# Kernel optimization log

Hardware: AMD Instinct MI355X
Metric: run time of the kernel (lower is better)

## Reference

```python
import jax, jax.numpy as jnp
import numpy as np

H, C = 2, 32  # heads, out_channels per head
NEG_SLOPE = 0.2


def gatv2_layer(h, src, dst, ea, W, b, We, att, bias, N):
    # shared lin_l = lin_r (share_weights=True)
    z = (h @ W + b).reshape(N, H, C)                      # [N,H,C]
    e = (ea @ We).reshape(-1, H, C)                        # [E',H,C]
    s = jax.nn.leaky_relu(z[dst] + z[src] + e, NEG_SLOPE)  # [E',H,C]
    alpha = jnp.einsum('ehc,hc->eh', s, att)               # [E',H]
    # segment softmax over destination neighborhoods
    m = jax.ops.segment_max(alpha, dst, num_segments=N)
    m = jnp.where(jnp.isfinite(m), m, 0.0)
    ex = jnp.exp(alpha - m[dst])
    denom = jax.ops.segment_sum(ex, dst, num_segments=N)
    a = ex / (denom[dst] + 1e-16)                          # [E',H]
    msg = (z[src] * a[:, :, None]).reshape(-1, H * C)      # [E',H*C]
    out = jax.ops.segment_sum(msg, dst, num_segments=N) + bias
    return out                                             # [N,H*C]


def setup_inputs() -> dict:
    key = jax.random.key(0)
    ks = jax.random.split(key, 16)
    N, E = 50000, 800000
    inp = {
        'x': jax.random.normal(ks[0], (N, 2), jnp.float32),
        'edge_index': jax.random.randint(ks[1], (2, E), 0, N, jnp.int64 if jax.config.jax_enable_x64 else jnp.int32).astype(jnp.int32),
        'edge_attr': jax.random.uniform(ks[2], (E, 2), jnp.float32),
        'dest_index': 123,
        'W0': jax.random.normal(ks[3], (2, 64), jnp.float32) * 0.5,
        'b0': jnp.zeros((64,), jnp.float32),
        'We0': jax.random.normal(ks[4], (2, 64), jnp.float32) * 0.5,
        'att0': jax.random.normal(ks[5], (H, C), jnp.float32) * 0.5,
        'bias0': jnp.zeros((64,), jnp.float32),
        'W1': jax.random.normal(ks[6], (64, 64), jnp.float32) * 0.125,
        'b1': jnp.zeros((64,), jnp.float32),
        'We1': jax.random.normal(ks[7], (2, 64), jnp.float32) * 0.5,
        'att1': jax.random.normal(ks[8], (H, C), jnp.float32) * 0.5,
        'bias1': jnp.zeros((64,), jnp.float32),
        'Wm1': jax.random.normal(ks[9], (194, 32), jnp.float32) * 0.07,
        'bm1': jnp.zeros((32,), jnp.float32),
        'Wm2': jax.random.normal(ks[10], (32, 1), jnp.float32) * 0.17,
        'bm2': jnp.zeros((1,), jnp.float32),
    }
    return inp


def reference(x, edge_index, edge_attr, dest_index,
              W0, b0, We0, att0, bias0,
              W1, b1, We1, att1, bias1,
              Wm1, bm1, Wm2, bm2):
    N = x.shape[0]
    # add self loops (fill_value='mean' for edge_attr)
    loops = jnp.arange(N, dtype=edge_index.dtype)
    src = jnp.concatenate([edge_index[0], loops])
    dst = jnp.concatenate([edge_index[1], loops])
    ea_sl = jnp.concatenate(
        [edge_attr, jnp.broadcast_to(edge_attr.mean(axis=0), (N, edge_attr.shape[1]))], axis=0)

    h = x
    h = jax.nn.elu(gatv2_layer(h, src, dst, ea_sl, W0, b0, We0, att0, bias0, N))
    h = jax.nn.elu(gatv2_layer(h, src, dst, ea_sl, W1, b1, We1, att1, bias1, N))

    goal = h[dest_index]                                   # [64]
    src_emb = h[edge_index[0]]                             # [E,64]
    dst_emb = h[edge_index[1]]                             # [E,64]
    goal_rep = jnp.broadcast_to(goal, (edge_index.shape[1], goal.shape[0]))
    edge_in = jnp.concatenate([src_emb, dst_emb, goal_rep, edge_attr], axis=-1)  # [E,194]
    hmlp = jax.nn.relu(edge_in @ Wm1 + bm1)
    logits = (hmlp @ Wm2 + bm2).squeeze(-1)                # [E]
    return logits
```

## Files before the change

### kernel.cpp

```cpp
#include <hip/hip_runtime.h>
#include <hip/hip_bf16.h>
#include <math.h>


typedef __attribute__((ext_vector_type(8))) short short8;
typedef __attribute__((ext_vector_type(4))) float f32x4;

#define BSH 7
#define CH 4096

template <int IMM>
__device__ __forceinline__ float swz(float x) {
    return __int_as_float(__builtin_amdgcn_ds_swizzle(__float_as_int(x), IMM));
}

template <int CTRL>
__device__ __forceinline__ float dpp_add(float p) {
    int t = __builtin_amdgcn_update_dpp(0, __float_as_int(p), CTRL, 0xF, 0xF, true);
    return p + __int_as_float(t);
}

__device__ __forceinline__ float head_reduce(float p) {
    p = dpp_add<0xB1>(p);
    p = dpp_add<0x4E>(p);
    p = dpp_add<0x141>(p);
    p = dpp_add<0x140>(p);
    p += swz<0x401F>(p);
    return p;
}

__device__ __forceinline__ short2 bsplit(float x) {
    unsigned u = __float_as_uint(x);
    short hi = (short)(u >> 16);
    float hif = __uint_as_float(u & 0xFFFF0000u);
    short lo = (short)(__float_as_uint(x - hif) >> 16);
    return make_short2(hi, lo);
}

__global__ void init_kernel(int* __restrict__ bucket_base, float* __restrict__ easum,
                            int nbuck) {
    int i = blockIdx.x * blockDim.x + threadIdx.x;
    if (i < nbuck) bucket_base[i] = 0;
    if (i < 2) easum[i] = 0.f;
}

__global__ __launch_bounds__(256) void easum_kernel(const float2* __restrict__ ea,
                                                    float* __restrict__ easum, int E) {
    __shared__ float r0[4], r1[4];
    int stride = gridDim.x * blockDim.x;
    float s0 = 0.f, s1 = 0.f;
    for (int e = blockIdx.x * blockDim.x + threadIdx.x; e < E; e += stride) {
        float2 v = ea[e];
        s0 += v.x; s1 += v.y;
    }
#pragma unroll
    for (int o = 32; o >= 1; o >>= 1) {
        s0 += __shfl_xor(s0, o);
        s1 += __shfl_xor(s1, o);
    }
    int wave = threadIdx.x >> 6;
    if ((threadIdx.x & 63) == 0) { r0[wave] = s0; r1[wave] = s1; }
    __syncthreads();
    if (threadIdx.x == 0) {
        atomicAdd(&easum[0], r0[0] + r0[1] + r0[2] + r0[3]);
        atomicAdd(&easum[1], r1[0] + r1[1] + r1[2] + r1[3]);
    }
}

__global__ __launch_bounds__(256) void bhist_kernel(const int* __restrict__ ei,
                                                    int* __restrict__ bucket_base,
                                                    int E, int EP, int nbuck) {
    extern __shared__ int lcnt[];
    int tid = threadIdx.x;
    for (int i = tid; i < nbuck; i += 256) lcnt[i] = 0;
    __syncthreads();
    int base = blockIdx.x * CH;
    int end = min(base + CH, EP);
    for (int i = base + tid; i < end; i += 256) {
        int d = (i < E) ? ei[E + i] : (i - E);
        atomicAdd(&lcnt[d >> BSH], 1);
    }
    __syncthreads();
    for (int i = tid; i < nbuck; i += 256) {
        int c = lcnt[i];
        if (c) atomicAdd(&bucket_base[i], c);
    }
}

__global__ __launch_bounds__(256) void bscan_kernel(int* __restrict__ bucket_base,
                                                    int* __restrict__ bucket_cursor,
                                                    int* __restrict__ row_ptr,
                                                    int N, int nbuck) {
    __shared__ int sm[256];
    int tid = threadIdx.x;
    int K = (nbuck + 255) / 256;
    int b0 = tid * K;
    int local = 0;
    for (int k = 0; k < K; ++k) {
        int b = b0 + k;
        if (b < nbuck) local += bucket_base[b];
    }
    sm[tid] = local;
    __syncthreads();
    for (int st = 1; st < 256; st <<= 1) {
        int v = sm[tid];
        int a = (tid >= st) ? sm[tid - st] : 0;
        __syncthreads();
        sm[tid] = v + a;
        __syncthreads();
    }
    int run = (tid == 0) ? 0 : sm[tid - 1];
    for (int k = 0; k < K; ++k) {
        int b = b0 + k;
        if (b < nbuck) {
            int c = bucket_base[b];
            bucket_base[b] = run;
            bucket_cursor[b] = run;
            run += c;
        }
    }
    if (tid == 255) {
        bucket_base[nbuck] = sm[255];
        row_ptr[N] = sm[255];
    }
}

__global__ __launch_bounds__(256) void phaseA_kernel(const int* __restrict__ ei,
                                                     const float2* __restrict__ ea,
                                                     const float* __restrict__ easum,
                                                     int* __restrict__ bucket_cursor,
                                                     float4* __restrict__ staged,
                                                     int E, int EP, int nbuck) {
    extern __shared__ int sm[];
    int* lcnt = sm;
    int* lbase = sm + nbuck;
    int tid = threadIdx.x;
    for (int i = tid; i < nbuck; i += 256) lcnt[i] = 0;
    __syncthreads();
    int base = blockIdx.x * CH;
    int end = min(base + CH, EP);
    for (int i = base + tid; i < end; i += 256) {
        int d = (i < E) ? ei[E + i] : (i - E);
        atomicAdd(&lcnt[d >> BSH], 1);
    }
    __syncthreads();
    for (int i = tid; i < nbuck; i += 256) {
        int c = lcnt[i];
        lbase[i] = c ? atomicAdd(&bucket_cursor[i], c) : 0;
        lcnt[i] = 0;
    }
    __syncthreads();
    float inv = 1.f / (float)E;
    float m0 = easum[0] * inv, m1 = easum[1] * inv;
    for (int i = base + tid; i < end; i += 256) {
        int s, d; float ex, ey;
        if (i < E) {
            s = ei[i]; d = ei[E + i];
            float2 v = ea[i]; ex = v.x; ey = v.y;
        } else {
            s = d = i - E; ex = m0; ey = m1;
        }
        int b = d >> BSH;
        int pos = lbase[b] + atomicAdd(&lcnt[b], 1);
        staged[pos] = make_float4(__int_as_float(s), ex, ey, __int_as_float(d));
    }
}

__global__ __launch_bounds__(256) void phaseB_kernel(const float4* __restrict__ staged,
                                                     const int* __restrict__ bucket_base,
                                                     int* __restrict__ row_ptr,
                                                     float4* __restrict__ recs, int N) {
    __shared__ int cnt128[128];
    __shared__ int offs[128];
    int b = blockIdx.x;
    int n0 = b << BSH;
    int tid = threadIdx.x;
    if (tid < 128) cnt128[tid] = 0;
    __syncthreads();
    int begs = bucket_base[b];
    int ends = bucket_base[b + 1];
    for (int i = begs + tid; i < ends; i += 256) {
        int d = __float_as_int(staged[i].w);
        atomicAdd(&cnt128[d - n0], 1);
    }
    __syncthreads();
    if (tid < 128) offs[tid] = cnt128[tid];
    __syncthreads();
    for (int st = 1; st < 128; st <<= 1) {
        int v = 0;
        if (tid < 128) {
            v = offs[tid];
            if (tid >= st) v += offs[tid - st];
        }
        __syncthreads();
        if (tid < 128) offs[tid] = v;
        __syncthreads();
    }
    if (tid < 128) {
        int excl = begs + offs[tid] - cnt128[tid];
        int node = n0 + tid;
        if (node < N) row_ptr[node] = excl;
        offs[tid] = excl;
    }
    __syncthreads();
    for (int i = begs + tid; i < ends; i += 256) {
        float4 r = staged[i];
        int d = __float_as_int(r.w);
        int pos = atomicAdd(&offs[d - n0], 1);
        recs[pos] = r;
    }
}

__global__ __launch_bounds__(512) void bfrag_kernel(const float* __restrict__ W1,
                                                    const float* __restrict__ Wm1,
                                                    short* __restrict__ BfW1,
                                                    short* __restrict__ BfWm) {
    int snt = threadIdx.x >> 6;
    int lane = threadIdx.x & 63;
    int s = snt >> 2, nt = snt & 3;
    int col = nt * 16 + (lane & 15);
    short* Bf = blockIdx.x == 0 ? BfW1 : BfWm;
#pragma unroll
    for (int j = 0; j < 8; ++j) {
        int k = s * 32 + (lane >> 4) * 8 + j;
        float v;
        if (blockIdx.x == 0) {
            v = W1[k * 64 + col];
        } else {
            v = (col < 32) ? Wm1[k * 32 + col] : Wm1[(64 + k) * 32 + (col - 32)];
        }
        short2 t = bsplit(v);
        Bf[(snt * 2 + 0) * 512 + lane * 8 + j] = t.x;
        Bf[(snt * 2 + 1) * 512 + lane * 8 + j] = t.y;
    }
}

__global__ __launch_bounds__(256) void mfma_gemm64(const float* __restrict__ h,
                                                   const short* __restrict__ Bf,
                                                   const float* __restrict__ bias,
                                                   float* __restrict__ out, int N) {
    int wave = threadIdx.x >> 6;
    int lane = threadIdx.x & 63;
    int n0 = blockIdx.x * 64 + wave * 16;
    if (n0 >= N) return;
    int m = lane & 15, quad = lane >> 4;
    int arow = n0 + m;
    if (arow > N - 1) arow = N - 1;

    f32x4 acc[4] = {{0.f, 0.f, 0.f, 0.f}, {0.f, 0.f, 0.f, 0.f},
                    {0.f, 0.f, 0.f, 0.f}, {0.f, 0.f, 0.f, 0.f}};
#pragma unroll
    for (int s = 0; s < 2; ++s) {
        const float* ap = h + (size_t)arow * 64 + s * 32 + quad * 8;
        float4 a0 = *(const float4*)ap;
        float4 a1 = *(const float4*)(ap + 4);
        short8 ahi, alo;
        short2 t;
        t = bsplit(a0.x); ahi[0] = t.x; alo[0] = t.y;
        t = bsplit(a0.y); ahi[1] = t.x; alo[1] = t.y;
        t = bsplit(a0.z); ahi[2] = t.x; alo[2] = t.y;
        t = bsplit(a0.w); ahi[3] = t.x; alo[3] = t.y;
        t = bsplit(a1.x); ahi[4] = t.x; alo[4] = t.y;
        t = bsplit(a1.y); ahi[5] = t.x; alo[5] = t.y;
        t = bsplit(a1.z); ahi[6] = t.x; alo[6] = t.y;
        t = bsplit(a1.w); ahi[7] = t.x; alo[7] = t.y;
#pragma unroll
        for (int nt = 0; nt < 4; ++nt) {
            const short* bp = Bf + ((s * 4 + nt) * 2) * 512 + lane * 8;
            short8 bhi = *(const short8*)bp;
            short8 blo = *(const short8*)(bp + 512);
            acc[nt] = __builtin_amdgcn_mfma_f32_16x16x32_bf16(ahi, bhi, acc[nt], 0, 0, 0);
            acc[nt] = __builtin_amdgcn_mfma_f32_16x16x32_bf16(ahi, blo, acc[nt], 0, 0, 0);
            acc[nt] = __builtin_amdgcn_mfma_f32_16x16x32_bf16(alo, bhi, acc[nt], 0, 0, 0);
        }
    }
#pragma unroll
    for (int nt = 0; nt < 4; ++nt) {
        int col = nt * 16 + m;
        float bj = bias ? bias[col] : 0.f;
#pragma unroll
        for (int r = 0; r < 4; ++r) {
            int orow = n0 + quad * 4 + r;
            if (orow < N) out[(size_t)orow * 64 + col] = acc[nt][r] + bj;
        }
    }
}

__global__ __launch_bounds__(256) void agg0_kernel(
    const float2* __restrict__ x, const float* __restrict__ W0,
    const float* __restrict__ b0, const int* __restrict__ row_ptr,
    const float4* __restrict__ recs,
    const float* __restrict__ We, const float* __restrict__ att,
    const float* __restrict__ bias, float* __restrict__ hout, int N) {
    int gtid = blockIdx.x * blockDim.x + threadIdx.x;
    int n = gtid >> 6;
    if (n >= N) return;
    n = __builtin_amdgcn_readfirstlane(n);
    int lane = threadIdx.x & 63;

    float W0a = W0[lane], W0b = W0[64 + lane], b0c = b0[lane];
    float We0 = We[lane], We1 = We[64 + lane];
    float attj = att[lane];
    float2 xn = x[n];
    float zn = fmaf(xn.x, W0a, fmaf(xn.y, W0b, b0c));

    int beg = row_ptr[n], end = row_ptr[n + 1];
    float ll[4] = {0.f, 0.f, 0.f, 0.f};
    float aa[4] = {0.f, 0.f, 0.f, 0.f};
    int i = beg;
    for (; i + 7 < end; i += 8) {
        float w[8], zsv[8];
#pragma unroll
        for (int k = 0; k < 8; ++k) {
            float4 r = recs[i + k];
            int s = __builtin_amdgcn_readfirstlane(__float_as_int(r.x));
            float2 xs = x[s];
            float zs = fmaf(xs.x, W0a, fmaf(xs.y, W0b, b0c));
            float sj = zn + zs + fmaf(r.y, We0, r.z * We1);
            sj = fmaxf(sj, 0.2f * sj);
            float alpha = head_reduce(sj * attj);
            w[k] = __expf(fminf(alpha, 60.f));
            zsv[k] = zs;
        }
#pragma unroll
        for (int k = 0; k < 8; ++k) {
            ll[k & 3] += w[k];
            aa[k & 3] = fmaf(w[k], zsv[k], aa[k & 3]);
        }
    }
    for (; i < end; ++i) {
        float4 r = recs[i];
        int s = __builtin_amdgcn_readfirstlane(__float_as_int(r.x));
        float2 xs = x[s];
        float zs = fmaf(xs.x, W0a, fmaf(xs.y, W0b, b0c));
        float sj = zn + zs + fmaf(r.y, We0, r.z * We1);
        sj = fmaxf(sj, 0.2f * sj);
        float alpha = head_reduce(sj * attj);
        float w = __expf(fminf(alpha, 60.f));
        ll[0] += w;
        aa[0] = fmaf(w, zs, aa[0]);
    }
    float l = (ll[0] + ll[1]) + (ll[2] + ll[3]);
    float acc = (aa[0] + aa[1]) + (aa[2] + aa[3]);
    float v = acc / (l + 1e-16f) + bias[lane];
    v = (v > 0.f) ? v : expm1f(v);
    hout[n * 64 + lane] = v;
}

__global__ __launch_bounds__(256) void agg1_kernel(
    const float* __restrict__ z, const int* __restrict__ row_ptr,
    const float4* __restrict__ recs,
    const float* __restrict__ We, const float* __restrict__ att,
    const float* __restrict__ bias, float* __restrict__ hout, int N) {
    int gtid = blockIdx.x * blockDim.x + threadIdx.x;
    int n = gtid >> 6;
    if (n >= N) return;
    n = __builtin_amdgcn_readfirstlane(n);
    int lane = threadIdx.x & 63;

    float We0 = We[lane], We1 = We[64 + lane];
    float attj = att[lane];
    float zn = z[n * 64 + lane];

    int beg = row_ptr[n], end = row_ptr[n + 1];
    float ll[4] = {0.f, 0.f, 0.f, 0.f};
    float aa[4] = {0.f, 0.f, 0.f, 0.f};
    int i = beg;
    for (; i + 7 < end; i += 8) {
        float w[8], zsv[8];
#pragma unroll
        for (int k = 0; k < 8; ++k) {
            float4 r = recs[i + k];
            int s = __builtin_amdgcn_readfirstlane(__float_as_int(r.x));
            float zs = z[s * 64 + lane];
            float sj = zn + zs + fmaf(r.y, We0, r.z * We1);
            sj = fmaxf(sj, 0.2f * sj);
            float alpha = head_reduce(sj * attj);
            w[k] = __expf(fminf(alpha, 60.f));
            zsv[k] = zs;
        }
#pragma unroll
        for (int k = 0; k < 8; ++k) {
            ll[k & 3] += w[k];
            aa[k & 3] = fmaf(w[k], zsv[k], aa[k & 3]);
        }
    }
    for (; i < end; ++i) {
        float4 r = recs[i];
        int s = __builtin_amdgcn_readfirstlane(__float_as_int(r.x));
        float zs = z[s * 64 + lane];
        float sj = zn + zs + fmaf(r.y, We0, r.z * We1);
        sj = fmaxf(sj, 0.2f * sj);
        float alpha = head_reduce(sj * attj);
        float w = __expf(fminf(alpha, 60.f));
        ll[0] += w;
        aa[0] = fmaf(w, zs, aa[0]);
    }
    float l = (ll[0] + ll[1]) + (ll[2] + ll[3]);
    float acc = (aa[0] + aa[1]) + (aa[2] + aa[3]);
    float v = acc / (l + 1e-16f) + bias[lane];
    v = (v > 0.f) ? v : expm1f(v);
    hout[n * 64 + lane] = v;
}

__global__ void gvec_kernel(const float* __restrict__ h, const float* __restrict__ Wm1,
                            const float* __restrict__ bm1, const int* __restrict__ dest,
                            float* __restrict__ gvec) {
    int q = threadIdx.x;
    if (q >= 32) return;
    int d = dest[0];
    float acc = bm1[q];
    for (int k = 0; k < 64; ++k)
        acc = fmaf(h[d * 64 + k], Wm1[(128 + k) * 32 + q], acc);
    gvec[q] = acc;
}

__global__ __launch_bounds__(256) void edge_mlp_kernel(
    const int* __restrict__ ei, const float2* __restrict__ ea,
    const float* __restrict__ hsd, const float* __restrict__ gvec,
    const float* __restrict__ WrowA, const float* __restrict__ WrowB,
    const float* __restrict__ Wm2, const float* __restrict__ bm2,
    float* __restrict__ out, int E) {
    int tid = blockIdx.x * blockDim.x + threadIdx.x;
    int e = tid >> 3;
    int j = tid & 7;
    if (e >= E) return;
    int s = ei[e], d = ei[E + e];
    float2 eav = ea[e];
    float4 a = *(const float4*)(hsd + (size_t)s * 64 + j * 4);
    float4 bv = *(const float4*)(hsd + (size_t)d * 64 + 32 + j * 4);
    float4 g = *(const float4*)(gvec + j * 4);
    float4 wa = *(const float4*)(WrowA + j * 4);
    float4 wb = *(const float4*)(WrowB + j * 4);
    float4 w2 = *(const float4*)(Wm2 + j * 4);
    float acc = 0.f, v;
    v = fmaf(eav.x, wa.x, fmaf(eav.y, wb.x, a.x + bv.x + g.x)); v = fmaxf(v, 0.f); acc = fmaf(v, w2.x, acc);
    v = fmaf(eav.x, wa.y, fmaf(eav.y, wb.y, a.y + bv.y + g.y)); v = fmaxf(v, 0.f); acc = fmaf(v, w2.y, acc);
    v = fmaf(eav.x, wa.z, fmaf(eav.y, wb.z, a.z + bv.z + g.z)); v = fmaxf(v, 0.f); acc = fmaf(v, w2.z, acc);
    v = fmaf(eav.x, wa.w, fmaf(eav.y, wb.w, a.w + bv.w + g.w)); v = fmaxf(v, 0.f); acc = fmaf(v, w2.w, acc);
    acc = dpp_add<0xB1>(acc);
    acc = dpp_add<0x4E>(acc);
    acc = dpp_add<0x141>(acc);
    if (j == 0) out[e] = acc + bm2[0];
}

extern "C" void kernel_launch(void* const* d_in, const int* in_sizes, int n_in,
                              void* d_out, int out_size, void* d_ws, size_t ws_size,
                              hipStream_t stream) {
    const float* x     = (const float*)d_in[0];
    const int*   ei    = (const int*)d_in[1];
    const float* ea    = (const float*)d_in[2];
    const int*   dest  = (const int*)d_in[3];
    const float* W0    = (const float*)d_in[4];
    const float* b0    = (const float*)d_in[5];
    const float* We0   = (const float*)d_in[6];
    const float* att0  = (const float*)d_in[7];
    const float* bias0 = (const float*)d_in[8];
    const float* W1    = (const float*)d_in[9];
    const float* b1    = (const float*)d_in[10];
    const float* We1   = (const float*)d_in[11];
    const float* att1  = (const float*)d_in[12];
    const float* bias1 = (const float*)d_in[13];
    const float* Wm1   = (const float*)d_in[14];
    const float* bm1   = (const float*)d_in[15];
    const float* Wm2   = (const float*)d_in[16];
    const float* bm2   = (const float*)d_in[17];

    const int N = in_sizes[0] / 2;
    const int E = in_sizes[1] / 2;
    const int EP = E + N;
    const int nbuck = (N + 127) >> BSH;
    const int nchunk = (EP + CH - 1) / CH;

    char* ws = (char*)d_ws;
    size_t off = 0;
    auto alloc = [&](size_t bytes) -> void* {
        void* p = ws + off;
        off += bytes;
        off = (off + 255) & ~(size_t)255;
        return p;
    };
    int*    bucket_base   = (int*)alloc((size_t)(nbuck + 1) * 4);
    int*    bucket_cursor = (int*)alloc((size_t)nbuck * 4);
    int*    row_ptr       = (int*)alloc((size_t)(N + 1) * 4);
    size_t  shared_bytes  = (size_t)EP * 16 > (size_t)N * 256 ? (size_t)EP * 16
                                                              : (size_t)N * 256;
    float4* staged        = (float4*)alloc(shared_bytes);
    float4* recs          = (float4*)alloc((size_t)EP * 16);
    float*  hbuf          = (float*)alloc((size_t)N * 64 * 4);
    float*  easum         = (float*)alloc(8);
    float*  gvec          = (float*)alloc(32 * 4);
    short*  BfW1          = (short*)alloc(8192 * 2);
    short*  BfWm          = (short*)alloc(8192 * 2);
    float*  zbuf          = (float*)staged;
    float*  hsd           = zbuf;

    dim3 blk(256);
    init_kernel<<<(nbuck + 255) / 256, blk, 0, stream>>>(bucket_base, easum, nbuck);
    easum_kernel<<<128, blk, 0, stream>>>((const float2*)ea, easum, E);
    bhist_kernel<<<nchunk, blk, (size_t)nbuck * 4, stream>>>(ei, bucket_base, E, EP, nbuck);
    bscan_kernel<<<1, blk, 0, stream>>>(bucket_base, bucket_cursor, row_ptr, N, nbuck);
    phaseA_kernel<<<nchunk, blk, (size_t)nbuck * 8, stream>>>(ei, (const float2*)ea, easum,
                                                              bucket_cursor, staged, E, EP, nbuck);
    phaseB_kernel<<<nbuck, blk, 0, stream>>>(staged, bucket_base, row_ptr, recs, N);
    bfrag_kernel<<<2, 512, 0, stream>>>(W1, Wm1, BfW1, BfWm);
    agg0_kernel<<<(N * 64 + 255) / 256, blk, 0, stream>>>((const float2*)x, W0, b0,
                                                          row_ptr, recs,
                                                          We0, att0, bias0, hbuf, N);
    mfma_gemm64<<<(N + 63) / 64, blk, 0, stream>>>(hbuf, BfW1, b1, zbuf, N);
    agg1_kernel<<<(N * 64 + 255) / 256, blk, 0, stream>>>(zbuf, row_ptr, recs,
                                                          We1, att1, bias1, hbuf, N);
    gvec_kernel<<<1, 64, 0, stream>>>(hbuf, Wm1, bm1, dest, gvec);
    mfma_gemm64<<<(N + 63) / 64, blk, 0, stream>>>(hbuf, BfWm, (const float*)nullptr, hsd, N);
    edge_mlp_kernel<<<((size_t)E * 8 + 255) / 256, blk, 0, stream>>>(
        ei, (const float2*)ea, hsd, gvec,
        Wm1 + 192 * 32, Wm1 + 193 * 32, Wm2, bm2, (float*)d_out, E);
}
```

Before: 293.0 us.

## Precompute per-edge attention weights in edge-parallel kernels and fuse setup launches

```diff
diff --git a/kernel.cpp b/kernel.cpp
--- a/kernel.cpp
+++ b/kernel.cpp
@@ -18,15 +18,6 @@
 __device__ __forceinline__ float dpp_add(float p) {
     int t = __builtin_amdgcn_update_dpp(0, __float_as_int(p), CTRL, 0xF, 0xF, true);
     return p + __int_as_float(t);
-}
-
-__device__ __forceinline__ float head_reduce(float p) {
-    p = dpp_add<0xB1>(p);
-    p = dpp_add<0x4E>(p);
-    p = dpp_add<0x141>(p);
-    p = dpp_add<0x140>(p);
-    p += swz<0x401F>(p);
-    return p;
 }
 
 __device__ __forceinline__ short2 bsplit(float x) {
@@ -37,19 +28,49 @@
     return make_short2(hi, lo);
 }
 
-__global__ void init_kernel(int* __restrict__ bucket_base, float* __restrict__ easum,
-                            int nbuck) {
-    int i = blockIdx.x * blockDim.x + threadIdx.x;
-    if (i < nbuck) bucket_base[i] = 0;
-    if (i < 2) easum[i] = 0.f;
-}
-
-__global__ __launch_bounds__(256) void easum_kernel(const float2* __restrict__ ea,
-                                                    float* __restrict__ easum, int E) {
+__global__ __launch_bounds__(512) void setup_kernel(const float* __restrict__ W1,
+                                                    const float* __restrict__ Wm1,
+                                                    short* __restrict__ BfW1,
+                                                    short* __restrict__ BfWm,
+                                                    int* __restrict__ bucket_base,
+                                                    float* __restrict__ easum, int nbuck) {
+    if (blockIdx.x == 2) {
+        for (int i = threadIdx.x; i <= nbuck; i += 512) bucket_base[i] = 0;
+        if (threadIdx.x < 2) easum[threadIdx.x] = 0.f;
+        return;
+    }
+    int snt = threadIdx.x >> 6;
+    int lane = threadIdx.x & 63;
+    int s = snt >> 2, nt = snt & 3;
+    int col = nt * 16 + (lane & 15);
+    short* Bf = blockIdx.x == 0 ? BfW1 : BfWm;
+#pragma unroll
+    for (int j = 0; j < 8; ++j) {
+        int k = s * 32 + (lane >> 4) * 8 + j;
+        float v;
+        if (blockIdx.x == 0) {
+            v = W1[k * 64 + col];
+        } else {
+            v = (col < 32) ? Wm1[k * 32 + col] : Wm1[(64 + k) * 32 + (col - 32)];
+        }
+        short2 t = bsplit(v);
+        Bf[(snt * 2 + 0) * 512 + lane * 8 + j] = t.x;
+        Bf[(snt * 2 + 1) * 512 + lane * 8 + j] = t.y;
+    }
+}
+
+__global__ __launch_bounds__(256) void pre_kernel(const int* __restrict__ ei,
+                                                  const float2* __restrict__ ea,
+                                                  int* __restrict__ bucket_base,
+                                                  float* __restrict__ easum,
+                                                  int E, int EP, int nbuck) {
+    extern __shared__ int lcnt[];
     __shared__ float r0[4], r1[4];
-    int stride = gridDim.x * blockDim.x;
+    int tid = threadIdx.x;
+    for (int i = tid; i < nbuck; i += 256) lcnt[i] = 0;
     float s0 = 0.f, s1 = 0.f;
-    for (int e = blockIdx.x * blockDim.x + threadIdx.x; e < E; e += stride) {
+    int estride = gridDim.x * 256;
+    for (int e = blockIdx.x * 256 + tid; e < E; e += estride) {
         float2 v = ea[e];
         s0 += v.x; s1 += v.y;
     }
@@ -58,21 +79,8 @@
         s0 += __shfl_xor(s0, o);
         s1 += __shfl_xor(s1, o);
     }
-    int wave = threadIdx.x >> 6;
-    if ((threadIdx.x & 63) == 0) { r0[wave] = s0; r1[wave] = s1; }
-    __syncthreads();
-    if (threadIdx.x == 0) {
-        atomicAdd(&easum[0], r0[0] + r0[1] + r0[2] + r0[3]);
-        atomicAdd(&easum[1], r1[0] + r1[1] + r1[2] + r1[3]);
-    }
-}
-
-__global__ __launch_bounds__(256) void bhist_kernel(const int* __restrict__ ei,
-                                                    int* __restrict__ bucket_base,
-                                                    int E, int EP, int nbuck) {
-    extern __shared__ int lcnt[];
-    int tid = threadIdx.x;
-    for (int i = tid; i < nbuck; i += 256) lcnt[i] = 0;
+    int wave = tid >> 6;
+    if ((tid & 63) == 0) { r0[wave] = s0; r1[wave] = s1; }
     __syncthreads();
     int base = blockIdx.x * CH;
     int end = min(base + CH, EP);
@@ -81,6 +89,10 @@
         atomicAdd(&lcnt[d >> BSH], 1);
     }
     __syncthreads();
+    if (tid == 0) {
+        atomicAdd(&easum[0], r0[0] + r0[1] + r0[2] + r0[3]);
+        atomicAdd(&easum[1], r1[0] + r1[1] + r1[2] + r1[3]);
+    }
     for (int i = tid; i < nbuck; i += 256) {
         int c = lcnt[i];
         if (c) atomicAdd(&bucket_base[i], c);
@@ -211,208 +223,269 @@
     }
 }
 
-__global__ __launch_bounds__(512) void bfrag_kernel(const float* __restrict__ W1,
-                                                    const float* __restrict__ Wm1,
-                                                    short* __restrict__ BfW1,
-                                                    short* __restrict__ BfWm) {
-    int snt = threadIdx.x >> 6;
+__global__ __launch_bounds__(256) void wgt1_kernel(const float* __restrict__ z,
+                                                   const float4* __restrict__ recs,
+                                                   const float* __restrict__ We,
+                                                   const float* __restrict__ att,
+                                                   float4* __restrict__ wbuf, int EP) {
     int lane = threadIdx.x & 63;
-    int s = snt >> 2, nt = snt & 3;
-    int col = nt * 16 + (lane & 15);
-    short* Bf = blockIdx.x == 0 ? BfW1 : BfWm;
+    int m = lane & 15, quad = lane >> 4;
+    int c0 = quad * 8, c1 = 32 + c0;
+    float w0a[8], w1a[8], ata[8], w0b[8], w1b[8], atb[8];
 #pragma unroll
     for (int j = 0; j < 8; ++j) {
-        int k = s * 32 + (lane >> 4) * 8 + j;
-        float v;
-        if (blockIdx.x == 0) {
-            v = W1[k * 64 + col];
-        } else {
-            v = (col < 32) ? Wm1[k * 32 + col] : Wm1[(64 + k) * 32 + (col - 32)];
-        }
-        short2 t = bsplit(v);
-        Bf[(snt * 2 + 0) * 512 + lane * 8 + j] = t.x;
-        Bf[(snt * 2 + 1) * 512 + lane * 8 + j] = t.y;
-    }
-}
-
-__global__ __launch_bounds__(256) void mfma_gemm64(const float* __restrict__ h,
-                                                   const short* __restrict__ Bf,
-                                                   const float* __restrict__ bias,
-                                                   float* __restrict__ out, int N) {
-    int wave = threadIdx.x >> 6;
+        w0a[j] = We[c0 + j];  w1a[j] = We[64 + c0 + j];  ata[j] = att[c0 + j];
+        w0b[j] = We[c1 + j];  w1b[j] = We[64 + c1 + j];  atb[j] = att[c1 + j];
+    }
+    int ntiles = (EP + 15) >> 4;
+    int wid = (blockIdx.x * blockDim.x + threadIdx.x) >> 6;
+    int nw = (gridDim.x * blockDim.x) >> 6;
+    for (int t = wid; t < ntiles; t += nw) {
+        int e = t * 16 + m;
+        int ec = e < EP ? e : EP - 1;
+        float4 r = recs[ec];
+        int s = __float_as_int(r.x);
+        int d = __float_as_int(r.w);
+        const float* zs = z + (size_t)s * 64;
+        const float* zd = z + (size_t)d * 64;
+        float4 sa0 = *(const float4*)(zs + c0), sa1 = *(const float4*)(zs + c0 + 4);
+        float4 sb0 = *(const float4*)(zs + c1), sb1 = *(const float4*)(zs + c1 + 4);
+        float4 da0 = *(const float4*)(zd + c0), da1 = *(const float4*)(zd + c0 + 4);
+        float4 db0 = *(const float4*)(zd + c1), db1 = *(const float4*)(zd + c1 + 4);
+        float sva[8] = {sa0.x, sa0.y, sa0.z, sa0.w, sa1.x, sa1.y, sa1.z, sa1.w};
+        float svb[8] = {sb0.x, sb0.y, sb0.z, sb0.w, sb1.x, sb1.y, sb1.z, sb1.w};
+        float dva[8] = {da0.x, da0.y, da0.z, da0.w, da1.x, da1.y, da1.z, da1.w};
+        float dvb[8] = {db0.x, db0.y, db0.z, db0.w, db1.x, db1.y, db1.z, db1.w};
+        float P0 = 0.f, P1 = 0.f;
+#pragma unroll
+        for (int j = 0; j < 8; ++j) {
+            float t0 = dva[j] + sva[j] + fmaf(r.y, w0a[j], r.z * w1a[j]);
+            t0 = fmaxf(t0, 0.2f * t0);
+            P0 = fmaf(t0, ata[j], P0);
+            float t1 = dvb[j] + svb[j] + fmaf(r.y, w0b[j], r.z * w1b[j]);
+            t1 = fmaxf(t1, 0.2f * t1);
+            P1 = fmaf(t1, atb[j], P1);
+        }
+        P0 += swz<0x401F>(P0);
+        P1 += swz<0x401F>(P1);
+        P0 += __shfl_xor(P0, 32);
+        P1 += __shfl_xor(P1, 32);
+        float w0 = __expf(fminf(P0, 60.f));
+        float w1 = __expf(fminf(P1, 60.f));
+        if (lane < 16 && e < EP) wbuf[e] = make_float4(w0, w1, r.x, 0.f);
+    }
+}
+
+__global__ __launch_bounds__(256) void wgt0_kernel(const float2* __restrict__ x,
+                                                   const float* __restrict__ W0,
+                                                   const float* __restrict__ b0,
+                                                   const float4* __restrict__ recs,
+                                                   const float* __restrict__ We,
+                                                   const float* __restrict__ att,
+                                                   float4* __restrict__ wbuf, int EP) {
     int lane = threadIdx.x & 63;
-    int n0 = blockIdx.x * 64 + wave * 16;
-    if (n0 >= N) return;
     int m = lane & 15, quad = lane >> 4;
-    int arow = n0 + m;
-    if (arow > N - 1) arow = N - 1;
-
-    f32x4 acc[4] = {{0.f, 0.f, 0.f, 0.f}, {0.f, 0.f, 0.f, 0.f},
-                    {0.f, 0.f, 0.f, 0.f}, {0.f, 0.f, 0.f, 0.f}};
-#pragma unroll
-    for (int s = 0; s < 2; ++s) {
-        const float* ap = h + (size_t)arow * 64 + s * 32 + quad * 8;
-        float4 a0 = *(const float4*)ap;
-        float4 a1 = *(const float4*)(ap + 4);
-        short8 ahi, alo;
-        short2 t;
-        t = bsplit(a0.x); ahi[0] = t.x; alo[0] = t.y;
-        t = bsplit(a0.y); ahi[1] = t.x; alo[1] = t.y;
-        t = bsplit(a0.z); ahi[2] = t.x; alo[2] = t.y;
-        t = bsplit(a0.w); ahi[3] = t.x; alo[3] = t.y;
-        t = bsplit(a1.x); ahi[4] = t.x; alo[4] = t.y;
-        t = bsplit(a1.y); ahi[5] = t.x; alo[5] = t.y;
-        t = bsplit(a1.z); ahi[6] = t.x; alo[6] = t.y;
-        t = bsplit(a1.w); ahi[7] = t.x; alo[7] = t.y;
-#pragma unroll
-        for (int nt = 0; nt < 4; ++nt) {
-            const short* bp = Bf + ((s * 4 + nt) * 2) * 512 + lane * 8;
-            short8 bhi = *(const short8*)bp;
-            short8 blo = *(const short8*)(bp + 512);
-            acc[nt] = __builtin_amdgcn_mfma_f32_16x16x32_bf16(ahi, bhi, acc[nt], 0, 0, 0);
-            acc[nt] = __builtin_amdgcn_mfma_f32_16x16x32_bf16(ahi, blo, acc[nt], 0, 0, 0);
-            acc[nt] = __builtin_amdgcn_mfma_f32_16x16x32_bf16(alo, bhi, acc[nt], 0, 0, 0);
-        }
-    }
-#pragma unroll
-    for (int nt = 0; nt < 4; ++nt) {
-        int col = nt * 16 + m;
-        float bj = bias ? bias[col] : 0.f;
-#pragma unroll
-        for (int r = 0; r < 4; ++r) {
-            int orow = n0 + quad * 4 + r;
-            if (orow < N) out[(size_t)orow * 64 + col] = acc[nt][r] + bj;
-        }
-    }
-}
-
-__global__ __launch_bounds__(256) void agg0_kernel(
-    const float2* __restrict__ x, const float* __restrict__ W0,
-    const float* __restrict__ b0, const int* __restrict__ row_ptr,
-    const float4* __restrict__ recs,
-    const float* __restrict__ We, const float* __restrict__ att,
-    const float* __restrict__ bias, float* __restrict__ hout, int N) {
+    int c0 = quad * 8, c1 = 32 + c0;
+    float w0a[8], w1a[8], ata[8], w0b[8], w1b[8], atb[8];
+    float Wxa[8], Wya[8], bca[8], Wxb[8], Wyb[8], bcb[8];
+#pragma unroll
+    for (int j = 0; j < 8; ++j) {
+        w0a[j] = We[c0 + j];  w1a[j] = We[64 + c0 + j];  ata[j] = att[c0 + j];
+        w0b[j] = We[c1 + j];  w1b[j] = We[64 + c1 + j];  atb[j] = att[c1 + j];
+        Wxa[j] = W0[c0 + j];  Wya[j] = W0[64 + c0 + j];  bca[j] = b0[c0 + j];
+        Wxb[j] = W0[c1 + j];  Wyb[j] = W0[64 + c1 + j];  bcb[j] = b0[c1 + j];
+    }
+    int ntiles = (EP + 15) >> 4;
+    int wid = (blockIdx.x * blockDim.x + threadIdx.x) >> 6;
+    int nw = (gridDim.x * blockDim.x) >> 6;
+    for (int t = wid; t < ntiles; t += nw) {
+        int e = t * 16 + m;
+        int ec = e < EP ? e : EP - 1;
+        float4 r = recs[ec];
+        int s = __float_as_int(r.x);
+        int d = __float_as_int(r.w);
+        float2 xs = x[s];
+        float2 xd = x[d];
+        float P0 = 0.f, P1 = 0.f;
+#pragma unroll
+        for (int j = 0; j < 8; ++j) {
+            float zs = fmaf(xs.x, Wxa[j], fmaf(xs.y, Wya[j], bca[j]));
+            float zd = fmaf(xd.x, Wxa[j], fmaf(xd.y, Wya[j], bca[j]));
+            float t0 = zd + zs + fmaf(r.y, w0a[j], r.z * w1a[j]);
+            t0 = fmaxf(t0, 0.2f * t0);
+            P0 = fmaf(t0, ata[j], P0);
+            float zs1 = fmaf(xs.x, Wxb[j], fmaf(xs.y, Wyb[j], bcb[j]));
+            float zd1 = fmaf(xd.x, Wxb[j], fmaf(xd.y, Wyb[j], bcb[j]));
+            float t1 = zd1 + zs1 + fmaf(r.y, w0b[j], r.z * w1b[j]);
+            t1 = fmaxf(t1, 0.2f * t1);
+            P1 = fmaf(t1, atb[j], P1);
+        }
+        P0 += swz<0x401F>(P0);
+        P1 += swz<0x401F>(P1);
+        P0 += __shfl_xor(P0, 32);
+        P1 += __shfl_xor(P1, 32);
+        float w0 = __expf(fminf(P0, 60.f));
+        float w1 = __expf(fminf(P1, 60.f));
+        if (lane < 16 && e < EP) wbuf[e] = make_float4(w0, w1, r.x, 0.f);
+    }
+}
+
+__global__ __launch_bounds__(256) void aggw1_kernel(const float* __restrict__ z,
+                                                    const int* __restrict__ row_ptr,
+                                                    const float4* __restrict__ wbuf,
+                                                    const float* __restrict__ bias,
+                                                    float* __restrict__ hout, int N) {
     int gtid = blockIdx.x * blockDim.x + threadIdx.x;
     int n = gtid >> 6;
     if (n >= N) return;
     n = __builtin_amdgcn_readfirstlane(n);
     int lane = threadIdx.x & 63;
-
-    float W0a = W0[lane], W0b = W0[64 + lane], b0c = b0[lane];
-    float We0 = We[lane], We1 = We[64 + lane];
-    float attj = att[lane];
-    float2 xn = x[n];
-    float zn = fmaf(xn.x, W0a, fmaf(xn.y, W0b, b0c));
-
+    int head = lane >> 5;
     int beg = row_ptr[n], end = row_ptr[n + 1];
     float ll[4] = {0.f, 0.f, 0.f, 0.f};
     float aa[4] = {0.f, 0.f, 0.f, 0.f};
     int i = beg;
-    for (; i + 7 < end; i += 8) {
-        float w[8], zsv[8];
+    for (; i + 8 <= end; i += 8) {
+        float w[8], zs[8];
 #pragma unroll
         for (int k = 0; k < 8; ++k) {
-            float4 r = recs[i + k];
-            int s = __builtin_amdgcn_readfirstlane(__float_as_int(r.x));
-            float2 xs = x[s];
-            float zs = fmaf(xs.x, W0a, fmaf(xs.y, W0b, b0c));
-            float sj = zn + zs + fmaf(r.y, We0, r.z * We1);
-            sj = fmaxf(sj, 0.2f * sj);
-            float alpha = head_reduce(sj * attj);
-            w[k] = __expf(fminf(alpha, 60.f));
-            zsv[k] = zs;
+            float4 r = wbuf[i + k];
+            int s = __builtin_amdgcn_readfirstlane(__float_as_int(r.z));
+            w[k] = head ? r.y : r.x;
+            zs[k] = z[(size_t)s * 64 + lane];
         }
 #pragma unroll
         for (int k = 0; k < 8; ++k) {
             ll[k & 3] += w[k];
-            aa[k & 3] = fmaf(w[k], zsv[k], aa[k & 3]);
+            aa[k & 3] = fmaf(w[k], zs[k], aa[k & 3]);
         }
     }
     for (; i < end; ++i) {
-        float4 r = recs[i];
-        int s = __builtin_amdgcn_readfirstlane(__float_as_int(r.x));
-        float2 xs = x[s];
-        float zs = fmaf(xs.x, W0a, fmaf(xs.y, W0b, b0c));
-        float sj = zn + zs + fmaf(r.y, We0, r.z * We1);
-        sj = fmaxf(sj, 0.2f * sj);
-        float alpha = head_reduce(sj * attj);
-        float w = __expf(fminf(alpha, 60.f));
+        float4 r = wbuf[i];
+        int s = __builtin_amdgcn_readfirstlane(__float_as_int(r.z));
+        float w = head ? r.y : r.x;
+        float zs = z[(size_t)s * 64 + lane];
         ll[0] += w;
         aa[0] = fmaf(w, zs, aa[0]);
     }
     float l = (ll[0] + ll[1]) + (ll[2] + ll[3]);
-    float acc = (aa[0] + aa[1]) + (aa[2] + aa[3]);
-    float v = acc / (l + 1e-16f) + bias[lane];
+    float a = (aa[0] + aa[1]) + (aa[2] + aa[3]);
+    float v = a / (l + 1e-16f) + bias[lane];
     v = (v > 0.f) ? v : expm1f(v);
-    hout[n * 64 + lane] = v;
-}
-
-__global__ __launch_bounds__(256) void agg1_kernel(
-    const float* __restrict__ z, const int* __restrict__ row_ptr,
-    const float4* __restrict__ recs,
-    const float* __restrict__ We, const float* __restrict__ att,
-    const float* __restrict__ bias, float* __restrict__ hout, int N) {
+    hout[(size_t)n * 64 + lane] = v;
+}
+
+__global__ __launch_bounds__(256) void aggw0_kernel(const float2* __restrict__ x,
+                                                    const float* __restrict__ W0,
+                                                    const float* __restrict__ b0,
+                                                    const int* __restrict__ row_ptr,
+                                                    const float4* __restrict__ wbuf,
+                                                    const float* __restrict__ bias,
+                                                    float* __restrict__ hout, int N) {
     int gtid = blockIdx.x * blockDim.x + threadIdx.x;
     int n = gtid >> 6;
     if (n >= N) return;
     n = __builtin_amdgcn_readfirstlane(n);
     int lane = threadIdx.x & 63;
-
-    float We0 = We[lane], We1 = We[64 + lane];
-    float attj = att[lane];
-    float zn = z[n * 64 + lane];
-
+    int head = lane >> 5;
+    float W0a = W0[lane], W0b = W0[64 + lane], b0c = b0[lane];
     int beg = row_ptr[n], end = row_ptr[n + 1];
     float ll[4] = {0.f, 0.f, 0.f, 0.f};
     float aa[4] = {0.f, 0.f, 0.f, 0.f};
     int i = beg;
-    for (; i + 7 < end; i += 8) {
-        float w[8], zsv[8];
+    for (; i + 8 <= end; i += 8) {
+        float w[8], zs[8];
 #pragma unroll
         for (int k = 0; k < 8; ++k) {
-            float4 r = recs[i + k];
-            int s = __builtin_amdgcn_readfirstlane(__float_as_int(r.x));
-            float zs = z[s * 64 + lane];
-            float sj = zn + zs + fmaf(r.y, We0, r.z * We1);
-            sj = fmaxf(sj, 0.2f * sj);
-            float alpha = head_reduce(sj * attj);
-            w[k] = __expf(fminf(alpha, 60.f));
-            zsv[k] = zs;
+            float4 r = wbuf[i + k];
+            int s = __builtin_amdgcn_readfirstlane(__float_as_int(r.z));
+            float2 xs = x[s];
+            w[k] = head ? r.y : r.x;
+            zs[k] = fmaf(xs.x, W0a, fmaf(xs.y, W0b, b0c));
         }
 #pragma unroll
         for (int k = 0; k < 8; ++k) {
             ll[k & 3] += w[k];
-            aa[k & 3] = fmaf(w[k], zsv[k], aa[k & 3]);
+            aa[k & 3] = fmaf(w[k], zs[k], aa[k & 3]);
         }
     }
     for (; i < end; ++i) {
-        float4 r = recs[i];
-        int s = __builtin_amdgcn_readfirstlane(__float_as_int(r.x));
-        float zs = z[s * 64 + lane];
-        float sj = zn + zs + fmaf(r.y, We0, r.z * We1);
-        sj = fmaxf(sj, 0.2f * sj);
-        float alpha = head_reduce(sj * attj);
-        float w = __expf(fminf(alpha, 60.f));
+        float4 r = wbuf[i];
+        int s = __builtin_amdgcn_readfirstlane(__float_as_int(r.z));
+        float2 xs = x[s];
+        float w = head ? r.y : r.x;
+        float zs = fmaf(xs.x, W0a, fmaf(xs.y, W0b, b0c));
         ll[0] += w;
         aa[0] = fmaf(w, zs, aa[0]);
     }
     float l = (ll[0] + ll[1]) + (ll[2] + ll[3]);
-    float acc = (aa[0] + aa[1]) + (aa[2] + aa[3]);
-    float v = acc / (l + 1e-16f) + bias[lane];
+    float a = (aa[0] + aa[1]) + (aa[2] + aa[3]);
+    float v = a / (l + 1e-16f) + bias[lane];
     v = (v > 0.f) ? v : expm1f(v);
-    hout[n * 64 + lane] = v;
-}
-
-__global__ void gvec_kernel(const float* __restrict__ h, const float* __restrict__ Wm1,
-                            const float* __restrict__ bm1, const int* __restrict__ dest,
-                            float* __restrict__ gvec) {
-    int q = threadIdx.x;
-    if (q >= 32) return;
-    int d = dest[0];
-    float acc = bm1[q];
-    for (int k = 0; k < 64; ++k)
-        acc = fmaf(h[d * 64 + k], Wm1[(128 + k) * 32 + q], acc);
-    gvec[q] = acc;
+    hout[(size_t)n * 64 + lane] = v;
+}
+
+__global__ __launch_bounds__(256) void mfma_gemm64(const float* __restrict__ h,
+                                                   const short* __restrict__ Bf,
+                                                   const float* __restrict__ bias,
+                                                   float* __restrict__ out, int N,
+                                                   const float* __restrict__ Wm1,
+                                                   const float* __restrict__ bm1,
+                                                   const int* __restrict__ dest,
+                                                   float* __restrict__ gv) {
+    int wave = threadIdx.x >> 6;
+    int lane = threadIdx.x & 63;
+    int n0 = blockIdx.x * 64 + wave * 16;
+    if (n0 < N) {
+        int m = lane & 15, quad = lane >> 4;
+        int arow = n0 + m;
+        if (arow > N - 1) arow = N - 1;
+        f32x4 acc[4] = {{0.f, 0.f, 0.f, 0.f}, {0.f, 0.f, 0.f, 0.f},
+                        {0.f, 0.f, 0.f, 0.f}, {0.f, 0.f, 0.f, 0.f}};
+#pragma unroll
+        for (int s = 0; s < 2; ++s) {
+            const float* ap = h + (size_t)arow * 64 + s * 32 + quad * 8;
+            float4 a0 = *(const float4*)ap;
+            float4 a1 = *(const float4*)(ap + 4);
+            short8 ahi, alo;
+            short2 t;
+            t = bsplit(a0.x); ahi[0] = t.x; alo[0] = t.y;
+            t = bsplit(a0.y); ahi[1] = t.x; alo[1] = t.y;
+            t = bsplit(a0.z); ahi[2] = t.x; alo[2] = t.y;
+            t = bsplit(a0.w); ahi[3] = t.x; alo[3] = t.y;
+            t = bsplit(a1.x); ahi[4] = t.x; alo[4] = t.y;
+            t = bsplit(a1.y); ahi[5] = t.x; alo[5] = t.y;
+            t = bsplit(a1.z); ahi[6] = t.x; alo[6] = t.y;
+            t = bsplit(a1.w); ahi[7] = t.x; alo[7] = t.y;
+#pragma unroll
+            for (int nt = 0; nt < 4; ++nt) {
+                const short* bp = Bf + ((s * 4 + nt) * 2) * 512 + lane * 8;
+                short8 bhi = *(const short8*)bp;
+                short8 blo = *(const short8*)(bp + 512);
+                acc[nt] = __builtin_amdgcn_mfma_f32_16x16x32_bf16(ahi, bhi, acc[nt], 0, 0, 0);
+                acc[nt] = __builtin_amdgcn_mfma_f32_16x16x32_bf16(ahi, blo, acc[nt], 0, 0, 0);
+                acc[nt] = __builtin_amdgcn_mfma_f32_16x16x32_bf16(alo, bhi, acc[nt], 0, 0, 0);
+            }
+        }
+#pragma unroll
+        for (int nt = 0; nt < 4; ++nt) {
+            int col = nt * 16 + m;
+            float bj = bias ? bias[col] : 0.f;
+#pragma unroll
+            for (int r = 0; r < 4; ++r) {
+                int orow = n0 + quad * 4 + r;
+                if (orow < N) out[(size_t)orow * 64 + col] = acc[nt][r] + bj;
+            }
+        }
+    }
+    if (gv && blockIdx.x == 0 && threadIdx.x < 32) {
+        int dd = dest[0];
+        int q = threadIdx.x;
+        float acc2 = bm1[q];
+        for (int k = 0; k < 64; ++k)
+            acc2 = fmaf(h[(size_t)dd * 64 + k], Wm1[(128 + k) * 32 + q], acc2);
+        gv[q] = acc2;
+    }
 }
 
 __global__ __launch_bounds__(256) void edge_mlp_kernel(
@@ -487,6 +560,7 @@
                                                               : (size_t)N * 256;
     float4* staged        = (float4*)alloc(shared_bytes);
     float4* recs          = (float4*)alloc((size_t)EP * 16);
+    float4* wbuf          = (float4*)alloc((size_t)EP * 16);
     float*  hbuf          = (float*)alloc((size_t)N * 64 * 4);
     float*  easum         = (float*)alloc(8);
     float*  gvec          = (float*)alloc(32 * 4);
@@ -496,22 +570,23 @@
     float*  hsd           = zbuf;
 
     dim3 blk(256);
-    init_kernel<<<(nbuck + 255) / 256, blk, 0, stream>>>(bucket_base, easum, nbuck);
-    easum_kernel<<<128, blk, 0, stream>>>((const float2*)ea, easum, E);
-    bhist_kernel<<<nchunk, blk, (size_t)nbuck * 4, stream>>>(ei, bucket_base, E, EP, nbuck);
+    setup_kernel<<<3, 512, 0, stream>>>(W1, Wm1, BfW1, BfWm, bucket_base, easum, nbuck);
+    pre_kernel<<<nchunk, blk, (size_t)nbuck * 4, stream>>>(ei, (const float2*)ea,
+                                                           bucket_base, easum, E, EP, nbuck);
     bscan_kernel<<<1, blk, 0, stream>>>(bucket_base, bucket_cursor, row_ptr, N, nbuck);
     phaseA_kernel<<<nchunk, blk, (size_t)nbuck * 8, stream>>>(ei, (const float2*)ea, easum,
                                                               bucket_cursor, staged, E, EP, nbuck);
     phaseB_kernel<<<nbuck, blk, 0, stream>>>(staged, bucket_base, row_ptr, recs, N);
-    bfrag_kernel<<<2, 512, 0, stream>>>(W1, Wm1, BfW1, BfWm);
-    agg0_kernel<<<(N * 64 + 255) / 256, blk, 0, stream>>>((const float2*)x, W0, b0,
-                                                          row_ptr, recs,
-                                                          We0, att0, bias0, hbuf, N);
-    mfma_gemm64<<<(N + 63) / 64, blk, 0, stream>>>(hbuf, BfW1, b1, zbuf, N);
-    agg1_kernel<<<(N * 64 + 255) / 256, blk, 0, stream>>>(zbuf, row_ptr, recs,
-                                                          We1, att1, bias1, hbuf, N);
-    gvec_kernel<<<1, 64, 0, stream>>>(hbuf, Wm1, bm1, dest, gvec);
-    mfma_gemm64<<<(N + 63) / 64, blk, 0, stream>>>(hbuf, BfWm, (const float*)nullptr, hsd, N);
+    wgt0_kernel<<<2048, blk, 0, stream>>>((const float2*)x, W0, b0, recs, We0, att0, wbuf, EP);
+    aggw0_kernel<<<(N * 64 + 255) / 256, blk, 0, stream>>>((const float2*)x, W0, b0,
+                                                           row_ptr, wbuf, bias0, hbuf, N);
+    mfma_gemm64<<<(N + 63) / 64, blk, 0, stream>>>(hbuf, BfW1, b1, zbuf, N,
+                                                   nullptr, nullptr, nullptr, nullptr);
+    wgt1_kernel<<<2048, blk, 0, stream>>>(zbuf, recs, We1, att1, wbuf, EP);
+    aggw1_kernel<<<(N * 64 + 255) / 256, blk, 0, stream>>>(zbuf, row_ptr, wbuf,
+                                                           bias1, hbuf, N);
+    mfma_gemm64<<<(N + 63) / 64, blk, 0, stream>>>(hbuf, BfWm, (const float*)nullptr, hsd, N,
+                                                   Wm1, bm1, dest, gvec);
     edge_mlp_kernel<<<((size_t)E * 8 + 255) / 256, blk, 0, stream>>>(
         ei, (const float2*)ea, hsd, gvec,
         Wm1 + 192 * 32, Wm1 + 193 * 32, Wm2, bm2, (float*)d_out, E);
```

New measurement: 339.3 us. +15.8%, slower.
